# Kernel tuning notes

Hardware: AMD Instinct MI355X
Metric: run time of the kernel (lower is better)

The kernel has to match this reference:

```python
import jax, jax.numpy as jnp
import numpy as np

F_IN, H, D, C, NCLS = 1024, 512, 256, 10, 4


def setup_inputs() -> dict:
    key = jax.random.key(0)
    ks = jax.random.split(key, 20)
    N = 32768
    x_path = jax.random.normal(ks[0], (N, F_IN), dtype=jnp.float32)
    cluster_id = jax.random.randint(ks[1], (N,), 0, C, dtype=jnp.int64)
    s1 = 1.0 / np.sqrt(F_IN)
    s2 = 1.0 / np.sqrt(H)
    s3 = 1.0 / np.sqrt(D)
    return {
        "x_path": x_path,
        "cluster_id": cluster_id,
        "W1": jax.random.normal(ks[2], (C, F_IN, H), dtype=jnp.float32) * s1,
        "b1": jnp.zeros((C, H), dtype=jnp.float32),
        "W2": jax.random.normal(ks[3], (C, H, H), dtype=jnp.float32) * s2,
        "b2": jnp.zeros((C, H), dtype=jnp.float32),
        "fc_W": jax.random.normal(ks[4], (H, H), dtype=jnp.float32) * s2,
        "fc_b": jnp.zeros((H,), dtype=jnp.float32),
        "a_W": jax.random.normal(ks[5], (H, D), dtype=jnp.float32) * s2,
        "a_b": jnp.zeros((D,), dtype=jnp.float32),
        "g_W": jax.random.normal(ks[6], (H, D), dtype=jnp.float32) * s2,
        "g_b": jnp.zeros((D,), dtype=jnp.float32),
        "c_W": jax.random.normal(ks[7], (D, 1), dtype=jnp.float32) * s3,
        "c_b": jnp.zeros((1,), dtype=jnp.float32),
        "rho_W": jax.random.normal(ks[8], (H, D), dtype=jnp.float32) * s2,
        "rho_b": jnp.zeros((D,), dtype=jnp.float32),
        "cls_W": jax.random.normal(ks[9], (D, NCLS), dtype=jnp.float32) * s3,
        "cls_b": jnp.zeros((NCLS,), dtype=jnp.float32),
    }


def reference(x_path, cluster_id, W1, b1, W2, b2, fc_W, fc_b, a_W, a_b,
              g_W, g_b, c_W, c_b, rho_W, rho_b, cls_W, cls_b):
    relu = jax.nn.relu
    means = []
    for i in range(C):  # fixed small set of clusters (structurally distinct MLPs)
        m = (cluster_id == i).astype(x_path.dtype)          # [N]
        y = relu(relu(x_path @ W1[i] + b1[i]) @ W2[i] + b2[i])  # [N, H]
        cnt = jnp.maximum(m.sum(), 1.0)
        means.append((y * m[:, None]).sum(axis=0) / cnt)    # [H] segment mean
    h_cluster = jnp.stack(means, axis=0)                    # [C, H]
    h = relu(h_cluster @ fc_W + fc_b)                       # [C, H]
    a = jnp.tanh(h @ a_W + a_b)                             # [C, D]
    g = jax.nn.sigmoid(h @ g_W + g_b)                       # [C, D]
    A = (a * g) @ c_W + c_b                                 # [C, 1]
    A = jax.nn.softmax(A.T, axis=1)                         # [1, C]
    h_path = A @ h                                          # [1, H]
    h_path = relu(h_path @ rho_W + rho_b).squeeze()         # [D]
    logits = (h_path @ cls_W + cls_b)[None, :]              # [1, NCLS]
    Y_hat = jnp.argmax(logits, axis=1, keepdims=True)       # [1, 1]
    hazards = jax.nn.sigmoid(logits)
    S = jnp.cumprod(1.0 - hazards, axis=1)
    return hazards, S, Y_hat
```

## Files before the change

kernel.cpp:

```cpp
#include <hip/hip_runtime.h>
#include <hip/hip_fp16.h>
#include <math.h>

#define FIN 1024
#define H 512
#define DD 256
#define NCLS 4
#define MAXC 64

#define TMM 32
#define WCOLS 40

#define WS_TOFF 1088
#define WS_NZ   1408
#define WS_SUMS 1536

typedef _Float16 f16x8 __attribute__((ext_vector_type(8)));
typedef _Float16 f16x4 __attribute__((ext_vector_type(4)));
typedef _Float16 f16x2 __attribute__((ext_vector_type(2)));
typedef float    f32x4 __attribute__((ext_vector_type(4)));

__global__ void detect_kernel(const int* __restrict__ cid32, int* flag, int n) {
    int i = blockIdx.x * blockDim.x + threadIdx.x;
    bool p = (i < n) && (i & 1) && (cid32[i] != 0);
    unsigned long long m = __ballot(p);
    if (p && ((threadIdx.x & 63) == (__ffsll(m) - 1))) atomicOr(flag, 1);
}

__device__ __forceinline__ int get_cid(const int* cid, int flag, int i) {
    return flag ? cid[i] : cid[2 * i];
}

__global__ void count_kernel(const int* __restrict__ cid, const int* __restrict__ flag,
                             int* counts, int n, int C) {
    __shared__ int lc[MAXC];
    int tid = threadIdx.x;
    if (tid < C) lc[tid] = 0;
    __syncthreads();
    int i = blockIdx.x * blockDim.x + tid;
    if (i < n) {
        int c = get_cid(cid, *flag, i);
        if ((unsigned)c < (unsigned)C) atomicAdd(&lc[c], 1);
    }
    __syncthreads();
    if (tid < C && lc[tid] > 0) atomicAdd(&counts[tid], lc[tid]);
}

__global__ void offsets_kernel(const int* __restrict__ counts, int* offs, int* toff,
                               int C, int tilesz) {
    if (threadIdx.x == 0 && blockIdx.x == 0) {
        int s = 0, ts = 0;
        offs[0] = 0; toff[0] = 0;
        for (int c = 0; c < C; c++) {
            s += counts[c];                          offs[c + 1] = s;
            ts += (counts[c] + tilesz - 1) / tilesz; toff[c + 1] = ts;
        }
    }
}

__global__ void compact_kernel(const int* __restrict__ cid, const int* __restrict__ flag,
                               const int* __restrict__ offs, int* cursor,
                               int* lists, int n, int C) {
    __shared__ int lc[MAXC], lbase[MAXC], lpos[MAXC];
    int tid = threadIdx.x;
    if (tid < C) { lc[tid] = 0; lpos[tid] = 0; }
    __syncthreads();
    int i = blockIdx.x * blockDim.x + tid;
    int c = -1;
    if (i < n) {
        int cc = get_cid(cid, *flag, i);
        if ((unsigned)cc < (unsigned)C) { c = cc; atomicAdd(&lc[c], 1); }
    }
    __syncthreads();
    if (tid < C && lc[tid] > 0) lbase[tid] = atomicAdd(&cursor[tid], lc[tid]);
    __syncthreads();
    if (c >= 0) {
        int p = atomicAdd(&lpos[c], 1);
        lists[offs[c] + lbase[c] + p] = i;
    }
}

__global__ __launch_bounds__(256) void xprep_kernel(
    const float* __restrict__ x, _Float16* __restrict__ x16, long long total8)
{
    long long stride = (long long)gridDim.x * 256;
    for (long long i = blockIdx.x * 256LL + threadIdx.x; i < total8; i += stride) {
        const float* p = x + i * 8;
        float4 a = *(const float4*)p;
        float4 b = *(const float4*)(p + 4);
        f16x8 v = { (_Float16)a.x, (_Float16)a.y, (_Float16)a.z, (_Float16)a.w,
                    (_Float16)b.x, (_Float16)b.y, (_Float16)b.z, (_Float16)b.w };
        *(f16x8*)(x16 + i * 8) = v;
    }
}


__device__ __forceinline__ int frag_off(int r, int g) {
    int blk = r >> 1;
    int slot = (((r & 1) << 2) | g) ^ (blk & 7);
    return blk * 128 + slot * 16;
}

__device__ __forceinline__ void inv_frag(int idx, int& r, int& g) {
    int blk = idx >> 3, slot = idx & 7;
    int s = slot ^ (blk & 7);
    r = (blk << 1) | (s >> 2);
    g = s & 3;
}

__device__ __forceinline__ void gload1k(const char* g, char* l) {
    __builtin_amdgcn_global_load_lds(
        (const __attribute__((address_space(1))) void*)g,
        (__attribute__((address_space(3))) void*)l, 16, 0, 0);
}

__device__ __forceinline__ void wprep_body(
    const float* __restrict__ W, _Float16* __restrict__ hi,
    _Float16* __restrict__ lo, int K, int b, float sw[32][132], int tid)
{
    int ktn = K >> 5;
    int c = b / (4 * ktn);
    int rem = b % (4 * ktn);
    int nb = rem / ktn, kt = rem % ktn;
    const float* Wc = W + (size_t)c * K * H + (size_t)(kt * 32) * H + nb * 128;
#pragma unroll
    for (int it = 0; it < 4; it++) {
        int id = it * 256 + tid;
        int r = id >> 5, c4 = (id & 31) * 4;
        *(float4*)&sw[r][c4] = *(const float4*)(Wc + (size_t)r * H + c4);
    }
    __syncthreads();
    size_t tile = ((size_t)(c * 4 + nb)) * ktn + kt;
    char* hp = (char*)hi + tile * 8192;
    char* lp = (char*)lo + tile * 8192;
#pragma unroll
    for (int it = 0; it < 2; it++) {
        int fi = it * 256 + tid;
        int cl = fi >> 2, g = fi & 3;
        f16x8 hv, lv;
#pragma unroll
        for (int e = 0; e < 8; e++) {
            float v = sw[g * 8 + e][cl];
            _Float16 h = (_Float16)v;
            hv[e] = h;
            lv[e] = (_Float16)(v - (float)h);
        }
        int off = frag_off(cl, g);
        *(f16x8*)(hp + off) = hv;
        *(f16x8*)(lp + off) = lv;
    }
}

__global__ __launch_bounds__(256) void wprep_both(
    const float* __restrict__ W1, _Float16* __restrict__ w1h, _Float16* __restrict__ w1l,
    const float* __restrict__ W2, _Float16* __restrict__ w2h, _Float16* __restrict__ w2l,
    int C)
{
    __shared__ float sw[32][132];
    int n1 = C * 4 * (FIN / 32);
    int b = blockIdx.x;
    int tid = threadIdx.x;
    if (b < n1) wprep_body(W1, w1h, w1l, FIN, b, sw, tid);
    else        wprep_body(W2, w2h, w2l, H, b - n1, sw, tid);
}

struct __align__(16) G1Smem {
    union {
        struct { _Float16 A[2][4096]; _Float16 Bh[2][4096]; _Float16 Bl[2][4096]; } s;
        _Float16 Ct[128][132];
    } u;
    int sIdx[128];
};

__global__ __launch_bounds__(256, 3) void gemm1(
    const _Float16* __restrict__ x16, const _Float16* __restrict__ zrow,
    const int* __restrict__ counts, const int* __restrict__ offs,
    const int* __restrict__ toff, const int* __restrict__ lists,
    const _Float16* __restrict__ wh, const _Float16* __restrict__ wl,
    const float* __restrict__ b1, _Float16* __restrict__ h1,
    int C, int nwg)
{
    int bid = blockIdx.x;
    {
        int q = nwg >> 3, r = nwg & 7, xcd = bid & 7, k = bid >> 3;
        bid = (xcd < r ? xcd * (q + 1) : r * (q + 1) + (xcd - r) * q) + k;
    }
    int ntile = toff[C];
    if (bid >= ntile * 4) return;
    int t = bid >> 2, nb = bid & 3;
    int c = 0;
    while (c + 1 < C && t >= toff[c + 1]) c++;
    int cnt = counts[c];
    int row0 = (t - toff[c]) * 128;

    __shared__ G1Smem sm;
    int tid = threadIdx.x;
    int lane = tid & 63;
    int wave = __builtin_amdgcn_readfirstlane(tid >> 6);
    if (tid < 128) {
        int r = row0 + tid;
        sm.sIdx[tid] = (r < cnt) ? lists[offs[c] + r] : -1;
    }
    __syncthreads();

    int ch = wave * 2;
    int rA0, gA0, rA1, gA1;
    inv_frag(ch * 64 + lane, rA0, gA0);
    inv_frag(ch * 64 + 64 + lane, rA1, gA1);
    int gi0 = sm.sIdx[rA0], gi1 = sm.sIdx[rA1];
    const char* srcA0 = (gi0 >= 0)
        ? (const char*)(x16 + (size_t)gi0 * FIN) + gA0 * 16
        : (const char*)zrow + gA0 * 16;
    const char* srcA1 = (gi1 >= 0)
        ? (const char*)(x16 + (size_t)gi1 * FIN) + gA1 * 16
        : (const char*)zrow + gA1 * 16;

    const char* gh = (const char*)wh + ((size_t)(c * 4 + nb) * 32) * 8192;
    const char* gl = (const char*)wl + ((size_t)(c * 4 + nb) * 32) * 8192;
    char* ldsA  = (char*)sm.u.s.A;
    char* ldsBh = (char*)sm.u.s.Bh;
    char* ldsBl = (char*)sm.u.s.Bl;

    int wr = wave >> 1, wq = wave & 1;
    int l15 = lane & 15, g = lane >> 4;

    f32x4 acc[4][4];
#pragma unroll
    for (int i = 0; i < 4; i++)
#pragma unroll
        for (int j = 0; j < 4; j++) acc[i][j] = (f32x4){0.f, 0.f, 0.f, 0.f};

    for (int kt2 = 0; kt2 < 16; kt2++) {
        __syncthreads();
        {
            const char* gsh = gh + (size_t)(kt2 * 2) * 8192 + ch * 1024 + lane * 16;
            const char* gsl = gl + (size_t)(kt2 * 2) * 8192 + ch * 1024 + lane * 16;
#pragma unroll
            for (int s = 0; s < 2; s++) {
                gload1k(srcA0 + s * 64, ldsA + s * 8192 + ch * 1024);
                gload1k(srcA1 + s * 64, ldsA + s * 8192 + ch * 1024 + 1024);
                gload1k(gsh + s * 8192,        ldsBh + s * 8192 + ch * 1024);
                gload1k(gsh + s * 8192 + 1024, ldsBh + s * 8192 + ch * 1024 + 1024);
                gload1k(gsl + s * 8192,        ldsBl + s * 8192 + ch * 1024);
                gload1k(gsl + s * 8192 + 1024, ldsBl + s * 8192 + ch * 1024 + 1024);
            }
            srcA0 += 128; srcA1 += 128;
        }
        __syncthreads();
#pragma unroll
        for (int s = 0; s < 2; s++) {
            f16x8 a[4], bh[4], bl[4];
#pragma unroll
            for (int fr = 0; fr < 4; fr++)
                a[fr] = *(const f16x8*)(ldsA + s * 8192 + frag_off(wr * 64 + fr * 16 + l15, g));
#pragma unroll
            for (int fc = 0; fc < 4; fc++) {
                int col = wq * 64 + fc * 16 + l15;
                bh[fc] = *(const f16x8*)(ldsBh + s * 8192 + frag_off(col, g));
                bl[fc] = *(const f16x8*)(ldsBl + s * 8192 + frag_off(col, g));
            }
#pragma unroll
            for (int fr = 0; fr < 4; fr++)
#pragma unroll
                for (int fc = 0; fc < 4; fc++) {
                    acc[fr][fc] = __builtin_amdgcn_mfma_f32_16x16x32_f16(a[fr], bh[fc], acc[fr][fc], 0, 0, 0);
                    acc[fr][fc] = __builtin_amdgcn_mfma_f32_16x16x32_f16(a[fr], bl[fc], acc[fr][fc], 0, 0, 0);
                }
        }
    }
    __syncthreads();
    const float* b1c = b1 + (size_t)c * H + nb * 128;
#pragma unroll
    for (int fc = 0; fc < 4; fc++) {
        int colL = wq * 64 + fc * 16 + l15;
        float bv = b1c[colL];
#pragma unroll
        for (int fr = 0; fr < 4; fr++)
#pragma unroll
            for (int j = 0; j < 4; j++) {
                int rowL = wr * 64 + fr * 16 + g * 4 + j;
                float v = acc[fr][fc][j] + bv;
                sm.u.Ct[rowL][colL] = (_Float16)(v > 0.f ? v : 0.f);
            }
    }
    __syncthreads();
    char* hout = (char*)h1 + ((size_t)t * 16 + nb * 4) * 8192;
#pragma unroll
    for (int ktl = 0; ktl < 4; ktl++)
#pragma unroll
        for (int it = 0; it < 2; it++) {
            int fi = it * 256 + tid;
            int rl = fi >> 2, gg = fi & 3;
            f16x8 v = *(const f16x8*)&sm.u.Ct[rl][ktl * 32 + gg * 8];
            *(f16x8*)(hout + (size_t)ktl * 8192 + frag_off(rl, gg)) = v;
        }
}

struct __align__(16) GSmem {
    union {
        struct { _Float16 A[2][4096]; _Float16 Bh[2][4096]; _Float16 Bl[2][4096]; } s;
        _Float16 Ct[128][132];
    } u;
    int sIdx[128];
};

__global__ __launch_bounds__(256, 3) void gemm1_reg(
    const float* __restrict__ x,
    const int* __restrict__ counts, const int* __restrict__ offs,
    const int* __restrict__ toff, const int* __restrict__ lists,
    const _Float16* __restrict__ wh, const _Float16* __restrict__ wl,
    const float* __restrict__ b1, _Float16* __restrict__ h1,
    int C, int nwg)
{
    int bid = blockIdx.x;
    {
        int q = nwg >> 3, r = nwg & 7, xcd = bid & 7, k = bid >> 3;
        bid = (xcd < r ? xcd * (q + 1) : r * (q + 1) + (xcd - r) * q) + k;
    }
    int ntile = toff[C];
    if (bid >= ntile * 4) return;
    int t = bid >> 2, nb = bid & 3;
    int c = 0;
    while (c + 1 < C && t >= toff[c + 1]) c++;
    int cnt = counts[c];
    int row0 = (t - toff[c]) * 128;

    __shared__ GSmem sm;
    int tid = threadIdx.x;
    int lane = tid & 63;
    int wave = __builtin_amdgcn_readfirstlane(tid >> 6);
    if (tid < 128) {
        int r = row0 + tid;
        sm.sIdx[tid] = (r < cnt) ? lists[offs[c] + r] : -1;
    }
    __syncthreads();

    int r0 = tid >> 2, g0 = tid & 3;
    int gi0 = sm.sIdx[r0], gi1 = sm.sIdx[64 + r0];
    const float* xp0 = x + (size_t)(gi0 < 0 ? 0 : gi0) * FIN + g0 * 8;
    const float* xp1 = x + (size_t)(gi1 < 0 ? 0 : gi1) * FIN + g0 * 8;
    int aoff0 = frag_off(r0, g0), aoff1 = frag_off(64 + r0, g0);

    const char* gh = (const char*)wh + ((size_t)(c * 4 + nb) * 32) * 8192;
    const char* gl = (const char*)wl + ((size_t)(c * 4 + nb) * 32) * 8192;
    char* ldsA  = (char*)sm.u.s.A;
    char* ldsBh = (char*)sm.u.s.Bh;
    char* ldsBl = (char*)sm.u.s.Bl;
    int ch = wave * 2;

    int wr = wave >> 1, wq = wave & 1;
    int l15 = lane & 15, g = lane >> 4;

    f32x4 acc[4][4];
#pragma unroll
    for (int i = 0; i < 4; i++)
#pragma unroll
        for (int j = 0; j < 4; j++) acc[i][j] = (f32x4){0.f, 0.f, 0.f, 0.f};

    {
        const char* gsh = gh + ch * 1024 + lane * 16;
        const char* gsl = gl + ch * 1024 + lane * 16;
        gload1k(gsh,        ldsBh + ch * 1024);
        gload1k(gsh + 1024, ldsBh + ch * 1024 + 1024);
        gload1k(gsl,        ldsBl + ch * 1024);
        gload1k(gsl + 1024, ldsBl + ch * 1024 + 1024);
        float4 v0a = make_float4(0.f,0.f,0.f,0.f), v0b = v0a, v1a = v0a, v1b = v0a;
        if (gi0 >= 0) { v0a = *(const float4*)xp0; v0b = *(const float4*)(xp0 + 4); }
        if (gi1 >= 0) { v1a = *(const float4*)xp1; v1b = *(const float4*)(xp1 + 4); }
        f16x8 a0 = { (_Float16)v0a.x, (_Float16)v0a.y, (_Float16)v0a.z, (_Float16)v0a.w,
                     (_Float16)v0b.x, (_Float16)v0b.y, (_Float16)v0b.z, (_Float16)v0b.w };
        f16x8 a1 = { (_Float16)v1a.x, (_Float16)v1a.y, (_Float16)v1a.z, (_Float16)v1a.w,
                     (_Float16)v1b.x, (_Float16)v1b.y, (_Float16)v1b.z, (_Float16)v1b.w };
        *(f16x8*)(ldsA + aoff0) = a0;
        *(f16x8*)(ldsA + aoff1) = a1;
        xp0 += 32; xp1 += 32;
    }
    __syncthreads();

    int cur = 0;
    for (int kt = 0; kt < 32; kt++) {
        int nxt = cur ^ 1;
        bool pf = kt < 31;
        float4 v0a = make_float4(0.f,0.f,0.f,0.f), v0b = v0a, v1a = v0a, v1b = v0a;
        if (pf) {
            const char* gsh = gh + (size_t)(kt + 1) * 8192 + ch * 1024 + lane * 16;
            const char* gsl = gl + (size_t)(kt + 1) * 8192 + ch * 1024 + lane * 16;
            gload1k(gsh,        ldsBh + nxt * 8192 + ch * 1024);
            gload1k(gsh + 1024, ldsBh + nxt * 8192 + ch * 1024 + 1024);
            gload1k(gsl,        ldsBl + nxt * 8192 + ch * 1024);
            gload1k(gsl + 1024, ldsBl + nxt * 8192 + ch * 1024 + 1024);
            if (gi0 >= 0) { v0a = *(const float4*)xp0; v0b = *(const float4*)(xp0 + 4); }
            if (gi1 >= 0) { v1a = *(const float4*)xp1; v1b = *(const float4*)(xp1 + 4); }
            xp0 += 32; xp1 += 32;
        }
        f16x8 a[4], bh[4], bl[4];
#pragma unroll
        for (int fr = 0; fr < 4; fr++)
            a[fr] = *(const f16x8*)(ldsA + cur * 8192 + frag_off(wr * 64 + fr * 16 + l15, g));
#pragma unroll
        for (int fc = 0; fc < 4; fc++) {
            int col = wq * 64 + fc * 16 + l15;
            bh[fc] = *(const f16x8*)(ldsBh + cur * 8192 + frag_off(col, g));
            bl[fc] = *(const f16x8*)(ldsBl + cur * 8192 + frag_off(col, g));
        }
#pragma unroll
        for (int fr = 0; fr < 4; fr++)
#pragma unroll
            for (int fc = 0; fc < 4; fc++) {
                acc[fr][fc] = __builtin_amdgcn_mfma_f32_16x16x32_f16(a[fr], bh[fc], acc[fr][fc], 0, 0, 0);
                acc[fr][fc] = __builtin_amdgcn_mfma_f32_16x16x32_f16(a[fr], bl[fc], acc[fr][fc], 0, 0, 0);
            }
        if (pf) {
            f16x8 a0 = { (_Float16)v0a.x, (_Float16)v0a.y, (_Float16)v0a.z, (_Float16)v0a.w,
                         (_Float16)v0b.x, (_Float16)v0b.y, (_Float16)v0b.z, (_Float16)v0b.w };
            f16x8 a1 = { (_Float16)v1a.x, (_Float16)v1a.y, (_Float16)v1a.z, (_Float16)v1a.w,
                         (_Float16)v1b.x, (_Float16)v1b.y, (_Float16)v1b.z, (_Float16)v1b.w };
            *(f16x8*)(ldsA + nxt * 8192 + aoff0) = a0;
            *(f16x8*)(ldsA + nxt * 8192 + aoff1) = a1;
        }
        __syncthreads();
        cur = nxt;
    }
    __syncthreads();
    const float* b1c = b1 + (size_t)c * H + nb * 128;
#pragma unroll
    for (int fc = 0; fc < 4; fc++) {
        int colL = wq * 64 + fc * 16 + l15;
        float bv = b1c[colL];
#pragma unroll
        for (int fr = 0; fr < 4; fr++)
#pragma unroll
            for (int j = 0; j < 4; j++) {
                int rowL = wr * 64 + fr * 16 + g * 4 + j;
                float v = acc[fr][fc][j] + bv;
                sm.u.Ct[rowL][colL] = (_Float16)(v > 0.f ? v : 0.f);
            }
    }
    __syncthreads();
    char* hout = (char*)h1 + ((size_t)t * 16 + nb * 4) * 8192;
#pragma unroll
    for (int ktl = 0; ktl < 4; ktl++)
#pragma unroll
        for (int it = 0; it < 2; it++) {
            int fi = it * 256 + tid;
            int rl = fi >> 2, gg = fi & 3;
            f16x8 v = *(const f16x8*)&sm.u.Ct[rl][ktl * 32 + gg * 8];
            *(f16x8*)(hout + (size_t)ktl * 8192 + frag_off(rl, gg)) = v;
        }
}

__global__ __launch_bounds__(256, 3) void gemm2(
    const _Float16* __restrict__ h1,
    const int* __restrict__ counts, const int* __restrict__ toff,
    const _Float16* __restrict__ wh, const _Float16* __restrict__ wl,
    const float* __restrict__ b2, double* __restrict__ sums,
    int C, int nwg)
{
    int bid = blockIdx.x;
    {
        int q = nwg >> 3, r = nwg & 7, xcd = bid & 7, k = bid >> 3;
        bid = (xcd < r ? xcd * (q + 1) : r * (q + 1) + (xcd - r) * q) + k;
    }
    int ntile = toff[C];
    if (bid >= ntile * 4) return;
    int t = bid >> 2, nb = bid & 3;
    int c = 0;
    while (c + 1 < C && t >= toff[c + 1]) c++;
    int cnt = counts[c];
    int row0 = (t - toff[c]) * 128;

    __shared__ alignas(16) _Float16 sA2[2][4096];
    __shared__ alignas(16) _Float16 sBh2[2][4096];
    __shared__ alignas(16) _Float16 sBl2[2][4096];

    int tid = threadIdx.x;
    int lane = tid & 63;
    int wave = __builtin_amdgcn_readfirstlane(tid >> 6);
    int wr = wave >> 1, wq = wave & 1;
    int l15 = lane & 15, g = lane >> 4;
    int ch = wave * 2;

    const char* gA = (const char*)h1 + (size_t)t * 16 * 8192;
    const char* gh = (const char*)wh + ((size_t)(c * 4 + nb) * 16) * 8192;
    const char* gl = (const char*)wl + ((size_t)(c * 4 + nb) * 16) * 8192;

    f32x4 acc[4][4];
#pragma unroll
    for (int i = 0; i < 4; i++)
#pragma unroll
        for (int j = 0; j < 4; j++) acc[i][j] = (f32x4){0.f, 0.f, 0.f, 0.f};

    for (int kt2 = 0; kt2 < 8; kt2++) {
        __syncthreads();
        {
            const char* ga  = gA + (size_t)(kt2 * 2) * 8192 + ch * 1024 + lane * 16;
            const char* gsh = gh + (size_t)(kt2 * 2) * 8192 + ch * 1024 + lane * 16;
            const char* gsl = gl + (size_t)(kt2 * 2) * 8192 + ch * 1024 + lane * 16;
#pragma unroll
            for (int s = 0; s < 2; s++) {
                gload1k(ga  + s * 8192,        (char*)sA2  + s * 8192 + ch * 1024);
                gload1k(ga  + s * 8192 + 1024, (char*)sA2  + s * 8192 + ch * 1024 + 1024);
                gload1k(gsh + s * 8192,        (char*)sBh2 + s * 8192 + ch * 1024);
                gload1k(gsh + s * 8192 + 1024, (char*)sBh2 + s * 8192 + ch * 1024 + 1024);
                gload1k(gsl + s * 8192,        (char*)sBl2 + s * 8192 + ch * 1024);
                gload1k(gsl + s * 8192 + 1024, (char*)sBl2 + s * 8192 + ch * 1024 + 1024);
            }
        }
        __syncthreads();
#pragma unroll
        for (int s = 0; s < 2; s++) {
            f16x8 a[4], bh[4], bl[4];
#pragma unroll
            for (int fr = 0; fr < 4; fr++)
                a[fr] = *(const f16x8*)((char*)sA2 + s * 8192 + frag_off(wr * 64 + fr * 16 + l15, g));
#pragma unroll
            for (int fc = 0; fc < 4; fc++) {
                int col = wq * 64 + fc * 16 + l15;
                bh[fc] = *(const f16x8*)((char*)sBh2 + s * 8192 + frag_off(col, g));
                bl[fc] = *(const f16x8*)((char*)sBl2 + s * 8192 + frag_off(col, g));
            }
#pragma unroll
            for (int fr = 0; fr < 4; fr++)
#pragma unroll
                for (int fc = 0; fc < 4; fc++) {
                    acc[fr][fc] = __builtin_amdgcn_mfma_f32_16x16x32_f16(a[fr], bh[fc], acc[fr][fc], 0, 0, 0);
                    acc[fr][fc] = __builtin_amdgcn_mfma_f32_16x16x32_f16(a[fr], bl[fc], acc[fr][fc], 0, 0, 0);
                }
        }
    }
    const float* b2c = b2 + (size_t)c * H + nb * 128;
    int rbound = cnt - row0;
    float psum[4];
#pragma unroll
    for (int fc = 0; fc < 4; fc++) {
        int colL = wq * 64 + fc * 16 + l15;
        float bv = b2c[colL];
        float s = 0.f;
#pragma unroll
        for (int fr = 0; fr < 4; fr++)
#pragma unroll
            for (int j = 0; j < 4; j++) {
                int rowL = wr * 64 + fr * 16 + g * 4 + j;
                float v = acc[fr][fc][j] + bv;
                v = v > 0.f ? v : 0.f;
                if (rowL < rbound) s += v;
            }
        psum[fc] = s;
    }
#pragma unroll
    for (int fc = 0; fc < 4; fc++) {
        psum[fc] += __shfl_xor(psum[fc], 16);
        psum[fc] += __shfl_xor(psum[fc], 32);
    }
    if (g == 0) {
#pragma unroll
        for (int fc = 0; fc < 4; fc++)
            atomicAdd(&sums[(size_t)c * H + nb * 128 + wq * 64 + fc * 16 + l15],
                      (double)psum[fc]);
    }
}

__global__ __launch_bounds__(256) void wsplit_kernel(
    const float* __restrict__ W, _Float16* __restrict__ hi,
    _Float16* __restrict__ lo, int K, int N)
{
    __shared__ float tile[64][65];
    int tid = threadIdx.x;
    int tilesN = N >> 6, tilesK = K >> 6;
    int b = blockIdx.x;
    int c = b / (tilesK * tilesN);
    int r = b % (tilesK * tilesN);
    int tk = r / tilesN, tn = r % tilesN;
    const float* Wc = W + (size_t)c * K * N;
    int k0 = tk << 6, n0 = tn << 6;
#pragma unroll
    for (int it = 0; it < 16; it++) {
        int id = it * 256 + tid;
        int kr = id >> 6, nc = id & 63;
        tile[kr][nc] = Wc[(size_t)(k0 + kr) * N + n0 + nc];
    }
    __syncthreads();
    _Float16* hic = hi + (size_t)c * N * K;
    _Float16* loc = lo + (size_t)c * N * K;
#pragma unroll
    for (int it = 0; it < 8; it++) {
        int id = it * 256 + tid;
        int nc = id >> 5, kp = (id & 31) * 2;
        float a0 = tile[kp][nc], a1 = tile[kp + 1][nc];
        _Float16 h0 = (_Float16)a0, h1v = (_Float16)a1;
        _Float16 l0 = (_Float16)(a0 - (float)h0);
        _Float16 l1 = (_Float16)(a1 - (float)h1v);
        size_t off = (size_t)(n0 + nc) * K + k0 + kp;
        f16x2 hv = {h0, h1v}, lv = {l0, l1};
        *(f16x2*)(hic + off) = hv;
        *(f16x2*)(loc + off) = lv;
    }
}

struct __align__(16) MfmaSmem {
    _Float16 sW[2][128][WCOLS];
    _Float16 sH[TMM][520];
    _Float16 sX[TMM][WCOLS];
    int      sIdx[TMM];
};

__global__ __launch_bounds__(256, 2) void mlp_mfma(
    const float* __restrict__ x,
    const int* __restrict__ counts, const int* __restrict__ offs,
    const int* __restrict__ toff, const int* __restrict__ lists,
    const _Float16* __restrict__ w1h, const _Float16* __restrict__ w1l,
    const _Float16* __restrict__ w2h, const _Float16* __restrict__ w2l,
    const float* __restrict__ b1, const float* __restrict__ b2,
    double* __restrict__ sums, int C, int nwg)
{
    int bid = blockIdx.x;
    {
        int q = nwg >> 3, r = nwg & 7, xcd = bid & 7, k = bid >> 3;
        bid = (xcd < r ? xcd * (q + 1) : r * (q + 1) + (xcd - r) * q) + k;
    }
    if (bid >= toff[C]) return;
    int c = 0;
    while (c + 1 < C && bid >= toff[c + 1]) c++;
    int t = bid - toff[c];
    int cnt = counts[c];
    int row0 = t * TMM;

    __shared__ MfmaSmem sm;
    int tid  = threadIdx.x;
    int lane = tid & 63, wave = tid >> 6;
    int wr = wave >> 1, wq = wave & 1;
    int l15 = lane & 15, g = lane >> 4;

    if (tid < TMM) {
        int r = row0 + tid;
        sm.sIdx[tid] = (r < cnt) ? lists[offs[c] + r] : -1;
    }

    const _Float16* w1hc = w1h + (size_t)c * FIN * H;
    const _Float16* w1lc = w1l + (size_t)c * FIN * H;
    const _Float16* w2hc = w2h + (size_t)c * H * H;
    const _Float16* w2lc = w2l + (size_t)c * H * H;
    const float* b1c = b1 + (size_t)c * H;
    const float* b2c = b2 + (size_t)c * H;

    int xr = tid >> 3;
    int xk = (tid & 7) * 4;
    int s_lc = tid >> 2;
    int s_kc = (tid & 3) * 8;

    for (int nb = 0; nb < H; nb += 128) {
        f32x4 acc[4];
#pragma unroll
        for (int f = 0; f < 4; f++) acc[f] = (f32x4){0.f, 0.f, 0.f, 0.f};

        for (int kk = 0; kk < FIN; kk += 32) {
            __syncthreads();
            {
                int gi = sm.sIdx[xr];
                float4 v = make_float4(0.f, 0.f, 0.f, 0.f);
                if (gi >= 0) v = *(const float4*)(x + (size_t)gi * FIN + kk + xk);
                f16x4 hv = { (_Float16)v.x, (_Float16)v.y, (_Float16)v.z, (_Float16)v.w };
                *(f16x4*)&sm.sX[xr][xk] = hv;
            }
            {
                const _Float16* ph = w1hc + (size_t)(nb + s_lc) * FIN + kk + s_kc;
                const _Float16* pl = w1lc + (size_t)(nb + s_lc) * FIN + kk + s_kc;
                *(f16x8*)&sm.sW[0][s_lc][s_kc]      = *(const f16x8*)ph;
                *(f16x8*)&sm.sW[0][64 + s_lc][s_kc] = *(const f16x8*)(ph + (size_t)64 * FIN);
                *(f16x8*)&sm.sW[1][s_lc][s_kc]      = *(const f16x8*)pl;
                *(f16x8*)&sm.sW[1][64 + s_lc][s_kc] = *(const f16x8*)(pl + (size_t)64 * FIN);
            }
            __syncthreads();
            f16x8 a = *(const f16x8*)&sm.sX[wr * 16 + l15][g * 8];
#pragma unroll
            for (int f = 0; f < 4; f++) {
                int lc = wq * 64 + f * 16 + l15;
                f16x8 bh = *(const f16x8*)&sm.sW[0][lc][g * 8];
                f16x8 bl = *(const f16x8*)&sm.sW[1][lc][g * 8];
                acc[f] = __builtin_amdgcn_mfma_f32_16x16x32_f16(a, bh, acc[f], 0, 0, 0);
                acc[f] = __builtin_amdgcn_mfma_f32_16x16x32_f16(a, bl, acc[f], 0, 0, 0);
            }
        }
#pragma unroll
        for (int f = 0; f < 4; f++) {
            int col = nb + wq * 64 + f * 16 + l15;
            float bv = b1c[col];
#pragma unroll
            for (int j = 0; j < 4; j++) {
                int row = wr * 16 + g * 4 + j;
                float v = acc[f][j] + bv;
                sm.sH[row][col] = (_Float16)(v > 0.f ? v : 0.f);
            }
        }
    }

    for (int nb = 0; nb < H; nb += 128) {
        f32x4 acc[4];
#pragma unroll
        for (int f = 0; f < 4; f++) acc[f] = (f32x4){0.f, 0.f, 0.f, 0.f};

        for (int kk = 0; kk < H; kk += 32) {
            __syncthreads();
            {
                const _Float16* ph = w2hc + (size_t)(nb + s_lc) * H + kk + s_kc;
                const _Float16* pl = w2lc + (size_t)(nb + s_lc) * H + kk + s_kc;
                *(f16x8*)&sm.sW[0][s_lc][s_kc]      = *(const f16x8*)ph;
                *(f16x8*)&sm.sW[0][64 + s_lc][s_kc] = *(const f16x8*)(ph + (size_t)64 * H);
                *(f16x8*)&sm.sW[1][s_lc][s_kc]      = *(const f16x8*)pl;
                *(f16x8*)&sm.sW[1][64 + s_lc][s_kc] = *(const f16x8*)(pl + (size_t)64 * H);
            }
            __syncthreads();
            f16x8 a = *(const f16x8*)&sm.sH[wr * 16 + l15][kk + g * 8];
#pragma unroll
            for (int f = 0; f < 4; f++) {
                int lc = wq * 64 + f * 16 + l15;
                f16x8 bh = *(const f16x8*)&sm.sW[0][lc][g * 8];
                f16x8 bl = *(const f16x8*)&sm.sW[1][lc][g * 8];
                acc[f] = __builtin_amdgcn_mfma_f32_16x16x32_f16(a, bh, acc[f], 0, 0, 0);
                acc[f] = __builtin_amdgcn_mfma_f32_16x16x32_f16(a, bl, acc[f], 0, 0, 0);
            }
        }
        float psum[4];
#pragma unroll
        for (int f = 0; f < 4; f++) {
            int col = nb + wq * 64 + f * 16 + l15;
            float bv = b2c[col];
            float s = 0.f;
#pragma unroll
            for (int j = 0; j < 4; j++) {
                int row = wr * 16 + g * 4 + j;
                float v = acc[f][j] + bv;
                v = v > 0.f ? v : 0.f;
                if (sm.sIdx[row] >= 0) s += v;
            }
            psum[f] = s;
        }
#pragma unroll
        for (int f = 0; f < 4; f++) {
            psum[f] += __shfl_xor(psum[f], 16);
            psum[f] += __shfl_xor(psum[f], 32);
        }
        if (g == 0) {
#pragma unroll
            for (int f = 0; f < 4; f++) {
                int col = nb + wq * 64 + f * 16 + l15;
                atomicAdd(&sums[(size_t)c * H + col], (double)psum[f]);
            }
        }
    }
}

__global__ __launch_bounds__(256) void row_mlp(
    const float* __restrict__ x, const int* __restrict__ cid,
    const int* __restrict__ flag,
    const float* __restrict__ W1, const float* __restrict__ b1,
    const float* __restrict__ W2, const float* __restrict__ b2,
    double* __restrict__ sums, int n, int C)
{
    int r = blockIdx.x;
    if (r >= n) return;
    int c = get_cid(cid, *flag, r);
    if ((unsigned)c >= (unsigned)C) return;

    __shared__ float sx[FIN];
    __shared__ float sh[H];
    int tid = threadIdx.x;

    for (int i = tid; i < FIN; i += 256) sx[i] = x[(size_t)r * FIN + i];
    __syncthreads();

    const float* W1c = W1 + (size_t)c * FIN * H;
    const float* b1c = b1 + (size_t)c * H;
    for (int col = tid; col < H; col += 256) {
        float acc = 0.f;
        for (int k = 0; k < FIN; k++) acc += sx[k] * W1c[(size_t)k * H + col];
        acc += b1c[col];
        sh[col] = acc > 0.f ? acc : 0.f;
    }
    __syncthreads();

    const float* W2c = W2 + (size_t)c * H * H;
    const float* b2c = b2 + (size_t)c * H;
    for (int col = tid; col < H; col += 256) {
        float acc = 0.f;
        for (int k = 0; k < H; k++) acc += sh[k] * W2c[(size_t)k * H + col];
        acc += b2c[col];
        float y = acc > 0.f ? acc : 0.f;
        atomicAdd(&sums[(size_t)c * H + col], (double)y);
    }
}

__global__ __launch_bounds__(128) void tailA_kernel(
    const int* __restrict__ counts, const double* __restrict__ sums,
    const float* __restrict__ fcW, const float* __restrict__ fcb,
    double* __restrict__ h_ws, int* __restrict__ nzflag)
{
    int b = blockIdx.x;
    int c = b >> 2, ch = b & 3;
    int tid = threadIdx.x;
    __shared__ double shc[H];
    double denom = fmax((double)counts[c], 1.0);
    double nz = 0.0;
    for (int i = tid; i < H; i += 128) {
        double v = sums[(size_t)c * H + i];
        nz += fabs(v);
        shc[i] = v / denom;
    }
    if (ch == 0) {
        if (__any(nz != 0.0) && (tid & 63) == 0) atomicOr(nzflag, 1);
    }
    __syncthreads();
    int col = ch * 128 + tid;
    double acc = 0.0;
#pragma unroll 16
    for (int k = 0; k < H; k++) acc += shc[k] * (double)fcW[k * H + col];
    acc += (double)fcb[col];
    h_ws[(size_t)c * H + col] = acc > 0.0 ? acc : 0.0;
}

__global__ __launch_bounds__(128) void tailB_kernel(
    const double* __restrict__ h_ws,
    const float* __restrict__ aW, const float* __restrict__ ab,
    const float* __restrict__ gW, const float* __restrict__ gb,
    double* __restrict__ ag_ws)
{
    int b = blockIdx.x;
    int c = b >> 1, dh = b & 1;
    int tid = threadIdx.x;
    __shared__ double sh[H];
    for (int i = tid; i < H; i += 128) sh[i] = h_ws[(size_t)c * H + i];
    __syncthreads();
    int d = dh * 128 + tid;
    double aa = (double)ab[d], gg = (double)gb[d];
#pragma unroll 8
    for (int k = 0; k < H; k++) {
        double hv = sh[k];
        aa += hv * (double)aW[k * DD + d];
        gg += hv * (double)gW[k * DD + d];
    }
    ag_ws[(size_t)c * DD + d] = tanh(aa) / (1.0 + exp(-gg));
}

__global__ __launch_bounds__(256) void tailC_kernel(
    const double* __restrict__ h_ws, const double* __restrict__ ag_ws,
    const float* __restrict__ cW, const float* __restrict__ cb,
    const float* __restrict__ rhoW, const float* __restrict__ rhob,
    const float* __restrict__ clsW, const float* __restrict__ clsb,
    const int* __restrict__ counts, const int* __restrict__ nzflag,
    const int* __restrict__ cid_raw, int n, int C,
    float* __restrict__ out)
{
    int tid = threadIdx.x;
    int lane = tid & 63, w = tid >> 6;
    __shared__ double sA[MAXC];
    __shared__ double shp[H];
    __shared__ double sr[DD];
    __shared__ double lgs[NCLS];

    for (int c = w; c < C; c += 4) {
        double acc = 0.0;
        for (int d = lane; d < DD; d += 64)
            acc += ag_ws[(size_t)c * DD + d] * (double)cW[d];
#pragma unroll
        for (int off = 32; off >= 1; off >>= 1) acc += __shfl_xor(acc, off);
        if (lane == 0) sA[c] = acc + (double)cb[0];
    }
    __syncthreads();
    if (tid == 0) {
        double m = sA[0];
        for (int c = 1; c < C; c++) m = fmax(m, sA[c]);
        double s = 0.0;
        for (int c = 0; c < C; c++) { sA[c] = exp(sA[c] - m); s += sA[c]; }
        for (int c = 0; c < C; c++) sA[c] /= s;
    }
    __syncthreads();
    for (int col = tid; col < H; col += 256) {
        double s = 0.0;
        for (int c = 0; c < C; c++) s += sA[c] * h_ws[(size_t)c * H + col];
        shp[col] = s;
    }
    __syncthreads();
    {
        int d = tid;
        double acc = 0.0;
#pragma unroll 16
        for (int k = 0; k < H; k++) acc += shp[k] * (double)rhoW[k * DD + d];
        acc += (double)rhob[d];
        sr[d] = acc > 0.0 ? acc : 0.0;
    }
    __syncthreads();
    for (int kk = w; kk < NCLS; kk += 4) {
        double acc = 0.0;
        for (int d = lane; d < DD; d += 64)
            acc += sr[d] * (double)clsW[d * NCLS + kk];
#pragma unroll
        for (int off = 32; off >= 1; off >>= 1) acc += __shfl_xor(acc, off);
        if (lane == 0) lgs[kk] = acc + (double)clsb[kk];
    }
    __syncthreads();
    if (tid == 0) {
        int am = 0;
        double best = lgs[0];
        double run = 1.0;
        for (int kk = 0; kk < NCLS; kk++) {
            if (lgs[kk] > best) { best = lgs[kk]; am = kk; }
            double hz = 1.0 / (1.0 + exp(-lgs[kk]));
            out[kk] = (float)hz;
            run *= (1.0 - hz);
            out[NCLS + kk] = (float)run;
        }
        long long cnt_total = 0;
        for (int c = 0; c < C; c++) cnt_total += counts[c];
        float yout;
        if (cnt_total == 0) {
            yout = 4.0e6f + (float)((cid_raw[0] & 0xFFF) + 4096 * (cid_raw[1] & 0xFFF));
        } else if (cnt_total != (long long)n) {
            yout = 2.0e6f + (float)cnt_total;
        } else if (*nzflag == 0) {
            yout = 3.0e6f;
        } else {
            yout = (float)am;
        }
        out[2 * NCLS] = yout;
    }
}

__global__ void diag_kernel(float* __restrict__ out, float code) {
    if (threadIdx.x == 0) {
        double run = 1.0;
        for (int kk = 0; kk < NCLS; kk++) {
            out[kk] = 0.5f;
            run *= 0.5;
            out[NCLS + kk] = (float)run;
        }
        out[2 * NCLS] = code;
    }
}

extern "C" void kernel_launch(void* const* d_in, const int* in_sizes, int n_in,
                              void* d_out, int out_size, void* d_ws, size_t ws_size,
                              hipStream_t stream) {
    const float* x    = (const float*)d_in[0];
    const int*   cid  = (const int*)d_in[1];
    const float* W1   = (const float*)d_in[2];
    const float* b1   = (const float*)d_in[3];
    const float* W2   = (const float*)d_in[4];
    const float* b2   = (const float*)d_in[5];
    const float* fcW  = (const float*)d_in[6];
    const float* fcb  = (const float*)d_in[7];
    const float* aW   = (const float*)d_in[8];
    const float* ab   = (const float*)d_in[9];
    const float* gW   = (const float*)d_in[10];
    const float* gb   = (const float*)d_in[11];
    const float* cW   = (const float*)d_in[12];
    const float* cb   = (const float*)d_in[13];
    const float* rhoW = (const float*)d_in[14];
    const float* rhob = (const float*)d_in[15];
    const float* clsW = (const float*)d_in[16];
    const float* clsb = (const float*)d_in[17];
    float* out = (float*)d_out;

    long long n = in_sizes[1];
    long long C = (in_sizes[7] > 0) ? (long long)in_sizes[3] / in_sizes[7] : 0;
    bool shapes_ok =
        n > 0 &&
        (long long)in_sizes[0] == n * FIN &&
        in_sizes[7] == H && in_sizes[9] == DD && in_sizes[17] == NCLS &&
        C >= 1 && C <= MAXC &&
        (long long)in_sizes[2] == C * FIN * H &&
        (long long)in_sizes[4] == C * H * H;

    size_t hws_off   = WS_SUMS + (size_t)C * H * 8;
    size_t agws_off  = hws_off + (size_t)C * H * 8;
    size_t lists_off = agws_off + (size_t)C * DD * 8;
    size_t wt_off    = (lists_off + (size_t)n * 4 + 255) & ~(size_t)255;
    size_t w1t_bytes = (size_t)C * H * FIN * 2;
    size_t w2t_bytes = (size_t)C * H * H * 2;
    size_t w1h_off   = wt_off;
    size_t w1l_off   = w1h_off + w1t_bytes;
    size_t w2h_off   = w1l_off + w1t_bytes;
    size_t w2l_off   = w2h_off + w2t_bytes;
    size_t h1_off    = (w2l_off + w2t_bytes + 255) & ~(size_t)255;
    int    nn = (int)n, CC = (int)C;
    int    ntile_ub  = (nn + 127) / 128 + CC;
    size_t h1_bytes  = (size_t)ntile_ub * 16 * 8192;
    size_t x16_off   = (h1_off + h1_bytes + 255) & ~(size_t)255;
    size_t x16_bytes = (size_t)n * FIN * 2;
    size_t zrow_off  = x16_off + x16_bytes;
    size_t ws_fullx  = zrow_off + 2048;
    size_t ws_full   = x16_off;
    size_t ws_mid    = h1_off;
    size_t ws_row    = lists_off;

    if (!shapes_ok) {
        diag_kernel<<<1, 64, 0, stream>>>(out, 7.0e6f + (float)(C >= 0 ? C : 0));
        return;
    }
    if (ws_size < ws_row) {
        diag_kernel<<<1, 64, 0, stream>>>(
            out, 6.0e6f + (float)(ws_size > 0 ? (ws_size >> 10) : 0));
        return;
    }

    char* ws = (char*)d_ws;
    int*    counts = (int*)ws;
    int*    flag   = (int*)(ws + 256);
    int*    cursor = (int*)(ws + 512);
    int*    offs   = (int*)(ws + 768);
    int*    toff   = (int*)(ws + WS_TOFF);
    int*    nzflag = (int*)(ws + WS_NZ);
    double* sums   = (double*)(ws + WS_SUMS);
    double* h_ws   = (double*)(ws + hws_off);
    double* ag_ws  = (double*)(ws + agws_off);
    int*    lists  = (int*)(ws + lists_off);
    _Float16* w1h  = (_Float16*)(ws + w1h_off);
    _Float16* w1l  = (_Float16*)(ws + w1l_off);
    _Float16* w2h  = (_Float16*)(ws + w2h_off);
    _Float16* w2l  = (_Float16*)(ws + w2l_off);
    _Float16* h1   = (_Float16*)(ws + h1_off);
    _Float16* x16  = (_Float16*)(ws + x16_off);
    _Float16* zrow = (_Float16*)(ws + zrow_off);

    int nb = (nn + 255) / 256;

    hipMemsetAsync(ws, 0, hws_off, stream);

    detect_kernel<<<nb, 256, 0, stream>>>(cid, flag, nn);
    count_kernel<<<nb, 256, 0, stream>>>(cid, flag, counts, nn, CC);

    if (ws_size >= ws_full) {
        offsets_kernel<<<1, 64, 0, stream>>>(counts, offs, toff, CC, 128);
        compact_kernel<<<nb, 256, 0, stream>>>(cid, flag, offs, cursor, lists, nn, CC);
        wprep_both<<<CC * 4 * (FIN / 32 + H / 32), 256, 0, stream>>>(
            W1, w1h, w1l, W2, w2h, w2l, CC);
        int grid = ntile_ub * 4;
        if (ws_size >= ws_fullx) {
            hipMemsetAsync(ws + zrow_off, 0, 2048, stream);
            long long total8 = n * (FIN / 8);
            xprep_kernel<<<2048, 256, 0, stream>>>(x, x16, total8);
            gemm1<<<grid, 256, 0, stream>>>(x16, zrow, counts, offs, toff, lists,
                                            w1h, w1l, b1, h1, CC, grid);
        } else {
            gemm1_reg<<<grid, 256, 0, stream>>>(x, counts, offs, toff, lists,
                                                w1h, w1l, b1, h1, CC, grid);
        }
        gemm2<<<grid, 256, 0, stream>>>(h1, counts, toff, w2h, w2l, b2,
                                        sums, CC, grid);
    } else if (ws_size >= ws_mid) {
        offsets_kernel<<<1, 64, 0, stream>>>(counts, offs, toff, CC, TMM);
        compact_kernel<<<nb, 256, 0, stream>>>(cid, flag, offs, cursor, lists, nn, CC);
        wsplit_kernel<<<CC * (FIN / 64) * (H / 64), 256, 0, stream>>>(W1, w1h, w1l, FIN, H);
        wsplit_kernel<<<CC * (H / 64) * (H / 64), 256, 0, stream>>>(W2, w2h, w2l, H, H);
        int nt = (nn + TMM - 1) / TMM + CC;
        mlp_mfma<<<nt, 256, 0, stream>>>(x, counts, offs, toff, lists,
                                         w1h, w1l, w2h, w2l, b1, b2,
                                         sums, CC, nt);
    } else {
        row_mlp<<<nn, 256, 0, stream>>>(x, cid, flag, W1, b1, W2, b2, sums, nn, CC);
    }

    tailA_kernel<<<CC * 4, 128, 0, stream>>>(counts, sums, fcW, fcb, h_ws, nzflag);
    tailB_kernel<<<CC * 2, 128, 0, stream>>>(h_ws, aW, ab, gW, gb, ag_ws);
    tailC_kernel<<<1, 256, 0, stream>>>(h_ws, ag_ws, cW, cb, rhoW, rhob,
                                        clsW, clsb, counts, nzflag, cid,
                                        nn, CC, out);
}
```

Baseline: 489.6 us.

## Pre-gather x into cluster-sorted fragment-tiled fp16 layout fused with weight prep

Replaces the flat fp32-to-fp16 conversion of x with a prep pass that gathers rows by cluster list and writes them directly in the swizzled per-tile fragment layout that gemm1 consumes. That pass is merged with the weight-split prep into one launch. gemm1 then streams A tiles contiguously, like the B tiles, with no index lookup, scattered row gathers or zero-row handling. This removes one kernel launch and the gather indirection inside the GEMM. In exchange the prep pass does the scattered reads and writes padded tiles, which adds some extra memory traffic for padding rows.

```diff
diff --git a/kernel.cpp b/kernel.cpp
--- a/kernel.cpp
+++ b/kernel.cpp
@@ -80,32 +80,11 @@
     }
 }
 
-__global__ __launch_bounds__(256) void xprep_kernel(
-    const float* __restrict__ x, _Float16* __restrict__ x16, long long total8)
-{
-    long long stride = (long long)gridDim.x * 256;
-    for (long long i = blockIdx.x * 256LL + threadIdx.x; i < total8; i += stride) {
-        const float* p = x + i * 8;
-        float4 a = *(const float4*)p;
-        float4 b = *(const float4*)(p + 4);
-        f16x8 v = { (_Float16)a.x, (_Float16)a.y, (_Float16)a.z, (_Float16)a.w,
-                    (_Float16)b.x, (_Float16)b.y, (_Float16)b.z, (_Float16)b.w };
-        *(f16x8*)(x16 + i * 8) = v;
-    }
-}
-
 
 __device__ __forceinline__ int frag_off(int r, int g) {
     int blk = r >> 1;
     int slot = (((r & 1) << 2) | g) ^ (blk & 7);
     return blk * 128 + slot * 16;
-}
-
-__device__ __forceinline__ void inv_frag(int idx, int& r, int& g) {
-    int blk = idx >> 3, slot = idx & 7;
-    int s = slot ^ (blk & 7);
-    r = (blk << 1) | (s >> 2);
-    g = s & 3;
 }
 
 __device__ __forceinline__ void gload1k(const char* g, char* l) {
@@ -149,6 +128,63 @@
         *(f16x8*)(hp + off) = hv;
         *(f16x8*)(lp + off) = lv;
     }
+}
+
+__device__ __forceinline__ void xtprep_body(
+    const float* __restrict__ x, _Float16* __restrict__ xt,
+    const int* __restrict__ counts, const int* __restrict__ offs,
+    const int* __restrict__ toff, const int* __restrict__ lists,
+    int C, int b2, int tid)
+{
+    int t = b2 >> 3, kg = b2 & 7;
+    int c = 0;
+    while (c + 1 < C && t >= toff[c + 1]) c++;
+    int cnt = counts[c];
+    int row0 = (t - toff[c]) * 128;
+    int r = tid & 127;
+    int ktl0 = tid >> 7;
+    int rg = row0 + r;
+    int gi = (t < toff[C] && rg < cnt) ? lists[offs[c] + rg] : -1;
+    const float* src = x + (size_t)(gi < 0 ? 0 : gi) * FIN + kg * 128;
+    char* dst = (char*)xt + ((size_t)t * 32 + kg * 4) * 8192;
+#pragma unroll
+    for (int q = 0; q < 2; q++) {
+        int ktl = ktl0 + q * 2;
+        f16x8 gr[4];
+        if (gi >= 0) {
+#pragma unroll
+            for (int g4 = 0; g4 < 4; g4++) {
+                float4 a = *(const float4*)(src + ktl * 32 + g4 * 8);
+                float4 b = *(const float4*)(src + ktl * 32 + g4 * 8 + 4);
+                gr[g4] = (f16x8){ (_Float16)a.x, (_Float16)a.y, (_Float16)a.z, (_Float16)a.w,
+                                  (_Float16)b.x, (_Float16)b.y, (_Float16)b.z, (_Float16)b.w };
+            }
+        } else {
+#pragma unroll
+            for (int g4 = 0; g4 < 4; g4++) gr[g4] = (f16x8){0,0,0,0,0,0,0,0};
+        }
+        char* d = dst + (size_t)ktl * 8192;
+#pragma unroll
+        for (int g4 = 0; g4 < 4; g4++)
+            *(f16x8*)(d + frag_off(r, g4)) = gr[g4];
+    }
+}
+
+__global__ __launch_bounds__(256) void prep_all(
+    const float* __restrict__ W1, _Float16* __restrict__ w1h, _Float16* __restrict__ w1l,
+    const float* __restrict__ W2, _Float16* __restrict__ w2h, _Float16* __restrict__ w2l,
+    const float* __restrict__ x, _Float16* __restrict__ xt,
+    const int* __restrict__ counts, const int* __restrict__ offs,
+    const int* __restrict__ toff, const int* __restrict__ lists, int C)
+{
+    __shared__ float sw[32][132];
+    int nW1 = C * 4 * (FIN / 32);
+    int nW2 = C * 4 * (H / 32);
+    int b = blockIdx.x, tid = threadIdx.x;
+    if (b < nW1)            wprep_body(W1, w1h, w1l, FIN, b, sw, tid);
+    else if (b < nW1 + nW2) wprep_body(W2, w2h, w2l, H, b - nW1, sw, tid);
+    else                    xtprep_body(x, xt, counts, offs, toff, lists, C,
+                                        b - nW1 - nW2, tid);
 }
 
 __global__ __launch_bounds__(256) void wprep_both(
@@ -169,13 +205,11 @@
         struct { _Float16 A[2][4096]; _Float16 Bh[2][4096]; _Float16 Bl[2][4096]; } s;
         _Float16 Ct[128][132];
     } u;
-    int sIdx[128];
 };
 
 __global__ __launch_bounds__(256, 3) void gemm1(
-    const _Float16* __restrict__ x16, const _Float16* __restrict__ zrow,
-    const int* __restrict__ counts, const int* __restrict__ offs,
-    const int* __restrict__ toff, const int* __restrict__ lists,
+    const _Float16* __restrict__ xt,
+    const int* __restrict__ toff,
     const _Float16* __restrict__ wh, const _Float16* __restrict__ wl,
     const float* __restrict__ b1, _Float16* __restrict__ h1,
     int C, int nwg)
@@ -190,40 +224,22 @@
     int t = bid >> 2, nb = bid & 3;
     int c = 0;
     while (c + 1 < C && t >= toff[c + 1]) c++;
-    int cnt = counts[c];
-    int row0 = (t - toff[c]) * 128;
 
     __shared__ G1Smem sm;
     int tid = threadIdx.x;
     int lane = tid & 63;
     int wave = __builtin_amdgcn_readfirstlane(tid >> 6);
-    if (tid < 128) {
-        int r = row0 + tid;
-        sm.sIdx[tid] = (r < cnt) ? lists[offs[c] + r] : -1;
-    }
-    __syncthreads();
-
     int ch = wave * 2;
-    int rA0, gA0, rA1, gA1;
-    inv_frag(ch * 64 + lane, rA0, gA0);
-    inv_frag(ch * 64 + 64 + lane, rA1, gA1);
-    int gi0 = sm.sIdx[rA0], gi1 = sm.sIdx[rA1];
-    const char* srcA0 = (gi0 >= 0)
-        ? (const char*)(x16 + (size_t)gi0 * FIN) + gA0 * 16
-        : (const char*)zrow + gA0 * 16;
-    const char* srcA1 = (gi1 >= 0)
-        ? (const char*)(x16 + (size_t)gi1 * FIN) + gA1 * 16
-        : (const char*)zrow + gA1 * 16;
-
+    int wr = wave >> 1, wq = wave & 1;
+    int l15 = lane & 15, g = lane >> 4;
+
+    const char* gA = (const char*)xt + (size_t)t * 32 * 8192;
     const char* gh = (const char*)wh + ((size_t)(c * 4 + nb) * 32) * 8192;
     const char* gl = (const char*)wl + ((size_t)(c * 4 + nb) * 32) * 8192;
     char* ldsA  = (char*)sm.u.s.A;
     char* ldsBh = (char*)sm.u.s.Bh;
     char* ldsBl = (char*)sm.u.s.Bl;
 
-    int wr = wave >> 1, wq = wave & 1;
-    int l15 = lane & 15, g = lane >> 4;
-
     f32x4 acc[4][4];
 #pragma unroll
     for (int i = 0; i < 4; i++)
@@ -233,18 +249,18 @@
     for (int kt2 = 0; kt2 < 16; kt2++) {
         __syncthreads();
         {
+            const char* ga  = gA + (size_t)(kt2 * 2) * 8192 + ch * 1024 + lane * 16;
             const char* gsh = gh + (size_t)(kt2 * 2) * 8192 + ch * 1024 + lane * 16;
             const char* gsl = gl + (size_t)(kt2 * 2) * 8192 + ch * 1024 + lane * 16;
 #pragma unroll
             for (int s = 0; s < 2; s++) {
-                gload1k(srcA0 + s * 64, ldsA + s * 8192 + ch * 1024);
-                gload1k(srcA1 + s * 64, ldsA + s * 8192 + ch * 1024 + 1024);
+                gload1k(ga  + s * 8192,        ldsA  + s * 8192 + ch * 1024);
+                gload1k(ga  + s * 8192 + 1024, ldsA  + s * 8192 + ch * 1024 + 1024);
                 gload1k(gsh + s * 8192,        ldsBh + s * 8192 + ch * 1024);
                 gload1k(gsh + s * 8192 + 1024, ldsBh + s * 8192 + ch * 1024 + 1024);
                 gload1k(gsl + s * 8192,        ldsBl + s * 8192 + ch * 1024);
                 gload1k(gsl + s * 8192 + 1024, ldsBl + s * 8192 + ch * 1024 + 1024);
             }
-            srcA0 += 128; srcA1 += 128;
         }
         __syncthreads();
 #pragma unroll
@@ -876,7 +892,7 @@
     __syncthreads();
     for (int col = tid; col < H; col += 256) {
         double s = 0.0;
-        for (int c = 0; c < C; c++) s += sA[c] * h_ws[(size_t)c * H + col];
+        for (int c = 0; c < C; c++) s += sA[c] * h_ws[c * H + col];
         shp[col] = s;
     }
     __syncthreads();
@@ -984,11 +1000,10 @@
     int    nn = (int)n, CC = (int)C;
     int    ntile_ub  = (nn + 127) / 128 + CC;
     size_t h1_bytes  = (size_t)ntile_ub * 16 * 8192;
-    size_t x16_off   = (h1_off + h1_bytes + 255) & ~(size_t)255;
-    size_t x16_bytes = (size_t)n * FIN * 2;
-    size_t zrow_off  = x16_off + x16_bytes;
-    size_t ws_fullx  = zrow_off + 2048;
-    size_t ws_full   = x16_off;
+    size_t xt_off    = (h1_off + h1_bytes + 255) & ~(size_t)255;
+    size_t xt_bytes  = (size_t)ntile_ub * 32 * 8192;
+    size_t ws_fullx  = xt_off + xt_bytes;
+    size_t ws_full   = xt_off;
     size_t ws_mid    = h1_off;
     size_t ws_row    = lists_off;
 
@@ -1018,8 +1033,7 @@
     _Float16* w2h  = (_Float16*)(ws + w2h_off);
     _Float16* w2l  = (_Float16*)(ws + w2l_off);
     _Float16* h1   = (_Float16*)(ws + h1_off);
-    _Float16* x16  = (_Float16*)(ws + x16_off);
-    _Float16* zrow = (_Float16*)(ws + zrow_off);
+    _Float16* xt   = (_Float16*)(ws + xt_off);
 
     int nb = (nn + 255) / 256;
 
@@ -1031,16 +1045,15 @@
     if (ws_size >= ws_full) {
         offsets_kernel<<<1, 64, 0, stream>>>(counts, offs, toff, CC, 128);
         compact_kernel<<<nb, 256, 0, stream>>>(cid, flag, offs, cursor, lists, nn, CC);
-        wprep_both<<<CC * 4 * (FIN / 32 + H / 32), 256, 0, stream>>>(
-            W1, w1h, w1l, W2, w2h, w2l, CC);
         int grid = ntile_ub * 4;
         if (ws_size >= ws_fullx) {
-            hipMemsetAsync(ws + zrow_off, 0, 2048, stream);
-            long long total8 = n * (FIN / 8);
-            xprep_kernel<<<2048, 256, 0, stream>>>(x, x16, total8);
-            gemm1<<<grid, 256, 0, stream>>>(x16, zrow, counts, offs, toff, lists,
-                                            w1h, w1l, b1, h1, CC, grid);
+            int nprep = CC * 4 * (FIN / 32 + H / 32) + ntile_ub * 8;
+            prep_all<<<nprep, 256, 0, stream>>>(W1, w1h, w1l, W2, w2h, w2l,
+                                                x, xt, counts, offs, toff, lists, CC);
+            gemm1<<<grid, 256, 0, stream>>>(xt, toff, w1h, w1l, b1, h1, CC, grid);
         } else {
+            wprep_both<<<CC * 4 * (FIN / 32 + H / 32), 256, 0, stream>>>(
+                W1, w1h, w1l, W2, w2h, w2l, CC);
             gemm1_reg<<<grid, 256, 0, stream>>>(x, counts, offs, toff, lists,
                                                 w1h, w1l, b1, h1, CC, grid);
         }
```

Measured after the change: 496.4 us. No clear change (+1.4%).
